# Kernel optimization log

Hardware: AMD Instinct MI355X
Metric: run time of the kernel (lower is better)

Reference implementation:

```python
import jax, jax.numpy as jnp
import numpy as np

B, S, HID = 2, 2048, 1024
H, D = 16, HID // 16  # heads, head_dim
ROPE_BASE = 10000.0


def setup_inputs() -> dict:
    key = jax.random.key(0)
    k1, k2, k3, k4 = jax.random.split(key, 4)
    scale = 1.0 / np.sqrt(HID)
    return {
        "hidden_states": jax.random.normal(k1, (B, S, HID), dtype=jnp.float32),
        "attention_mask": jnp.zeros((B, 1, 1, S), dtype=jnp.float32),
        "Wq": jax.random.normal(k2, (HID, HID), dtype=jnp.float32) * scale,
        "Wk": jax.random.normal(k3, (HID, HID), dtype=jnp.float32) * scale,
        "Wv": jax.random.normal(k4, (HID, HID), dtype=jnp.float32) * scale,
    }


def _rope_cos_sin(seq_len, dim, dtype):
    inv_freq = 1.0 / (ROPE_BASE ** (jnp.arange(0, dim, 2, dtype=jnp.float32) / dim))
    freqs = jnp.arange(seq_len, dtype=jnp.float32)[:, None] * inv_freq[None, :]  # (S, D/2)
    emb = jnp.concatenate([freqs, freqs], axis=-1)  # (S, D)
    return jnp.cos(emb).astype(dtype), jnp.sin(emb).astype(dtype)


def _rotate_half(x):
    x1, x2 = jnp.split(x, 2, axis=-1)
    return jnp.concatenate([-x2, x1], axis=-1)


def reference(hidden_states, attention_mask, Wq, Wk, Wv):
    b, s, _ = hidden_states.shape
    # QKV projections (no bias), split into heads: (b, H, s, D)
    def proj(W):
        return jnp.einsum('bse,de->bsd', hidden_states, W).reshape(b, s, H, D).transpose(0, 2, 1, 3)
    q, k, v = proj(Wq), proj(Wk), proj(Wv)
    # Rotary embedding on q, k over sequence positions
    cos, sin = _rope_cos_sin(s, D, hidden_states.dtype)  # (s, D)
    cos = cos[None, None]  # (1,1,s,D)
    sin = sin[None, None]
    q = q * cos + _rotate_half(q) * sin
    k = k * cos + _rotate_half(k) * sin
    # Scaled dot-product attention with additive mask
    scores = jnp.einsum('bhqd,bhkd->bhqk', q, k) / jnp.sqrt(jnp.asarray(D, hidden_states.dtype))
    scores = scores + attention_mask
    probs = jax.nn.softmax(scores, axis=-1)  # dropout p=0 (eval) -> identity
    ctx = jnp.einsum('bhqk,bhkd->bhqd', probs, v)
    return ctx.transpose(0, 2, 1, 3).reshape(b, s, H * D)
```

## Files before the change

kernel.cpp:

```cpp
#include <hip/hip_runtime.h>
#include <stdint.h>

typedef unsigned short u16;
typedef short bf16x8 __attribute__((ext_vector_type(8)));
typedef float f32x4 __attribute__((ext_vector_type(4)));

#define S_ 2048
#define HID_ 1024
#define H_ 16
#define D_ 64

#define LOG2E 1.4426950408889634f
#define SCALE_LOG2 0.18033688011112042f
#define MAXC_LOG2 11.541560327111707f

__device__ __forceinline__ u16 f2bf(float f) {
  uint32_t x = __builtin_bit_cast(uint32_t, f);
  uint32_t r = (x + 0x7fffu + ((x >> 16) & 1u)) >> 16;
  return (u16)r;
}
__device__ __forceinline__ uint32_t packbf2(float a, float b) {
  return (uint32_t)f2bf(a) | ((uint32_t)f2bf(b) << 16);
}
__device__ __forceinline__ uint32_t permpack(float a, float b) {
  return __builtin_amdgcn_perm(__builtin_bit_cast(uint32_t, b),
                               __builtin_bit_cast(uint32_t, a), 0x07060302u);
}

__device__ __forceinline__ void gl2lds16(const void* g, void* l) {
  __builtin_amdgcn_global_load_lds(
      (const __attribute__((address_space(1))) unsigned int*)g,
      (__attribute__((address_space(3))) unsigned int*)l, 16, 0, 0);
}

#define NX_ (1 << 20)
#define NW_ (1 << 18)
#define NROPE_ 65536
__global__ void prep_kernel(const float* __restrict__ X, const float* __restrict__ Wq,
                            const float* __restrict__ Wk, const float* __restrict__ Wv,
                            const float* __restrict__ mask, u16* __restrict__ Xb,
                            u16* __restrict__ Wqb, u16* __restrict__ Wkb,
                            u16* __restrict__ Wvb, float* __restrict__ cos_t,
                            float* __restrict__ sin_t, float* __restrict__ mask2) {
  int i = blockIdx.x * 256 + threadIdx.x;
  if (i < NX_ + 3 * NW_) {
    const float* src;
    u16* dst;
    int off;
    if (i < NX_) {
      src = X; dst = Xb; off = i;
    } else if (i < NX_ + NW_) {
      src = Wq; dst = Wqb; off = i - NX_;
    } else if (i < NX_ + 2 * NW_) {
      src = Wk; dst = Wkb; off = i - NX_ - NW_;
    } else {
      src = Wv; dst = Wvb; off = i - NX_ - 2 * NW_;
    }
    float4 v = ((const float4*)src)[off];
    uint2 packed;
    packed.x = packbf2(v.x, v.y);
    packed.y = packbf2(v.z, v.w);
    ((uint2*)dst)[off] = packed;
  } else if (i < NX_ + 3 * NW_ + NROPE_) {
    int t = i - (NX_ + 3 * NW_);
    int s = t >> 5, j = t & 31;
    float invf = powf(10000.0f, -(float)j * (1.0f / 32.0f));
    float ang = (float)s * invf;
    cos_t[t] = cosf(ang);
    sin_t[t] = sinf(ang);
  } else {
    int t = i - (NX_ + 3 * NW_ + NROPE_);
    mask2[t] = fmaf(mask[t], LOG2E, -MAXC_LOG2);
  }
}

__global__ __launch_bounds__(256) void qkv_gemm_kernel(
    const u16* __restrict__ X, const u16* __restrict__ Wq, const u16* __restrict__ Wk,
    const u16* __restrict__ Wv, const float* __restrict__ cos_t,
    const float* __restrict__ sin_t, u16* __restrict__ Q, u16* __restrict__ K,
    u16* __restrict__ Vt) {
  __shared__ char smem[65536];
  int tid = threadIdx.x;
  int lane = tid & 63, wave = tid >> 6;
  int wm = wave >> 1, wn = wave & 1;
  int quad = lane >> 4, l16 = lane & 15;
  int which = blockIdx.x >> 3;
  int nbase = (blockIdx.x & 7) * 128;
  int mbase = blockIdx.y * 128;
  const u16* W = (which == 0) ? Wq : (which == 1) ? Wk : Wv;

#pragma unroll
  for (int it = 0; it < 4; ++it) {
    int i = it * 256 + tid;
    int r = i >> 3, gs = i & 7, gsrc = gs ^ (r & 7);
    gl2lds16(X + (size_t)(mbase + r) * HID_ + gsrc * 8, smem + i * 16);
    gl2lds16(W + (size_t)(nbase + r) * HID_ + gsrc * 8, smem + 32768 + i * 16);
  }

  f32x4 acc[4][4] = {};

  for (int kk = 0; kk < 16; ++kk) {
    char* As = smem + (kk & 1) * 16384;
    char* Bs = smem + 32768 + (kk & 1) * 16384;
    __syncthreads();

    if (kk < 15) {
      int k0n = (kk + 1) * 64;
      char* An = smem + ((kk + 1) & 1) * 16384;
      char* Bn = smem + 32768 + ((kk + 1) & 1) * 16384;
#pragma unroll
      for (int it = 0; it < 4; ++it) {
        int i = it * 256 + tid;
        int r = i >> 3, gs = i & 7, gsrc = gs ^ (r & 7);
        gl2lds16(X + (size_t)(mbase + r) * HID_ + k0n + gsrc * 8, An + i * 16);
        gl2lds16(W + (size_t)(nbase + r) * HID_ + k0n + gsrc * 8, Bn + i * 16);
      }
    }

#pragma unroll
    for (int kh = 0; kh < 2; ++kh) {
      bf16x8 afrag[4], bfrag[4];
#pragma unroll
      for (int i4 = 0; i4 < 4; ++i4) {
        int r = wm * 64 + i4 * 16 + l16;
        int L = r * 8 + ((kh * 4 + quad) ^ (r & 7));
        afrag[i4] = *(const bf16x8*)(As + L * 16);
      }
#pragma unroll
      for (int j4 = 0; j4 < 4; ++j4) {
        int r = wn * 64 + j4 * 16 + l16;
        int L = r * 8 + ((kh * 4 + quad) ^ (r & 7));
        bfrag[j4] = *(const bf16x8*)(Bs + L * 16);
      }
      if (which == 2) {
#pragma unroll
        for (int i4 = 0; i4 < 4; ++i4)
#pragma unroll
          for (int j4 = 0; j4 < 4; ++j4)
            acc[i4][j4] = __builtin_amdgcn_mfma_f32_16x16x32_bf16(afrag[i4], bfrag[j4],
                                                                  acc[i4][j4], 0, 0, 0);
      } else {
#pragma unroll
        for (int i4 = 0; i4 < 4; ++i4)
#pragma unroll
          for (int j4 = 0; j4 < 4; ++j4)
            acc[i4][j4] = __builtin_amdgcn_mfma_f32_16x16x32_bf16(bfrag[j4], afrag[i4],
                                                                  acc[i4][j4], 0, 0, 0);
      }
    }
  }

  if (which == 2) {
#pragma unroll
    for (int i4 = 0; i4 < 4; ++i4)
#pragma unroll
      for (int j4 = 0; j4 < 4; ++j4) {
        int m = mbase + wm * 64 + i4 * 16 + quad * 4;
        int n = nbase + wn * 64 + j4 * 16 + l16;
        int b = m >> 11, s0 = m & 2047;
        int h = n >> 6, d = n & 63;
        uint2 pk;
        pk.x = packbf2(acc[i4][j4][0], acc[i4][j4][1]);
        pk.y = packbf2(acc[i4][j4][2], acc[i4][j4][3]);
        *(uint2*)(Vt + (((size_t)(b * H_ + h)) * D_ + d) * S_ + s0) = pk;
      }
  } else {
    u16* dst = (which == 0) ? Q : K;
#pragma unroll
    for (int i4 = 0; i4 < 4; ++i4)
#pragma unroll
      for (int j4 = 0; j4 < 2; ++j4) {
        int m = mbase + wm * 64 + i4 * 16 + l16;
        int n1 = nbase + wn * 64 + j4 * 16 + quad * 4;
        int b = m >> 11, s = m & 2047;
        int h = n1 >> 6, d1 = n1 & 63;
        float4 c4 = *(const float4*)(cos_t + s * 32 + d1);
        float4 s4 = *(const float4*)(sin_t + s * 32 + d1);
        float y1[4], y2[4];
#pragma unroll
        for (int r = 0; r < 4; ++r) {
          float cr = ((const float*)&c4)[r], sr = ((const float*)&s4)[r];
          float x1 = acc[i4][j4][r], x2 = acc[i4][j4 + 2][r];
          y1[r] = x1 * cr - x2 * sr;
          y2[r] = x2 * cr + x1 * sr;
        }
        size_t base = ((size_t)(b * H_ + h) * S_ + s) * D_;
        uint2 p1, p2;
        p1.x = packbf2(y1[0], y1[1]);
        p1.y = packbf2(y1[2], y1[3]);
        p2.x = packbf2(y2[0], y2[1]);
        p2.y = packbf2(y2[2], y2[3]);
        *(uint2*)(dst + base + d1) = p1;
        *(uint2*)(dst + base + d1 + 32) = p2;
      }
  }
}

__device__ __forceinline__ void pv_step(const char* Pr, const char* Vp, int quad, int l16,
                                        const bf16x8& ones, f32x4* o, f32x4& lacc) {
  bf16x8 p[2];
#pragma unroll
  for (int kh = 0; kh < 2; ++kh) {
    int c0 = kh * 8 + quad * 2;
    union { uint2 u[2]; bf16x8 v; } cv;
    cv.u[0] = *(const uint2*)(Pr + l16 * 128 + ((c0) ^ l16) * 8);
    cv.u[1] = *(const uint2*)(Pr + l16 * 128 + ((c0 + 1) ^ l16) * 8);
    p[kh] = cv.v;
  }
  lacc = __builtin_amdgcn_mfma_f32_16x16x32_bf16(p[0], ones, lacc, 0, 0, 0);
  lacc = __builtin_amdgcn_mfma_f32_16x16x32_bf16(p[1], ones, lacc, 0, 0, 0);
#pragma unroll
  for (int jd = 0; jd < 4; ++jd) {
    int r = jd * 16 + l16;
#pragma unroll
    for (int kh = 0; kh < 2; ++kh) {
      int L = r * 8 + ((kh * 4 + quad) ^ (r & 7));
      bf16x8 vf = *(const bf16x8*)(Vp + L * 16);
      o[jd] = __builtin_amdgcn_mfma_f32_16x16x32_bf16(p[kh], vf, o[jd], 0, 0, 0);
    }
  }
}

__global__ __launch_bounds__(512, 4) void flash_kernel(
    const u16* __restrict__ Q, const u16* __restrict__ K, const u16* __restrict__ Vt,
    const float* __restrict__ mask2, float* __restrict__ out) {
  __shared__ char smem[65536];
  int tid = threadIdx.x, wave = tid >> 6;
  int lane = tid & 63;
  int quad = lane >> 4, l16 = lane & 15;
  int bh = blockIdx.y, b = bh >> 4, h = bh & 15;
  int qbase = blockIdx.x * 128;
  int qw = qbase + wave * 16;
  char* Pw = smem + 49152 + wave * 2048;
  const float* m2row = mask2 + b * S_;
  const u16* Kbase = K + (size_t)bh * S_ * D_;
  const u16* Vbase = Vt + (size_t)bh * D_ * S_;

  bf16x8 qfrag[2];
  {
    const u16* qp = Q + ((size_t)bh * S_ + qw + l16) * D_ + quad * 8;
    qfrag[0] = *(const bf16x8*)qp;
    qfrag[1] = *(const bf16x8*)(qp + 32);
  }
  bf16x8 ones;
#pragma unroll
  for (int j = 0; j < 8; ++j) ones[j] = (short)0x3f80;

  f32x4 o[4] = {};
  f32x4 lacc = {};

  {
    int i = tid;
    int r = i >> 3, gs = i & 7, gsrc = gs ^ (r & 7);
    gl2lds16(Kbase + (size_t)r * D_ + gsrc * 8, smem + i * 16);
    gl2lds16(Vbase + (size_t)r * S_ + gsrc * 8, smem + 8192 + i * 16);
  }
  float4 mv[4];
#pragma unroll
  for (int jt = 0; jt < 4; ++jt) mv[jt] = *(const float4*)(m2row + jt * 16 + quad * 4);

  for (int kt = 0; kt < 32; ++kt) {
    char* Ks = smem + (kt % 3) * 16384;
    __syncthreads();

    if (kt < 31) {
      char* Kn = smem + ((kt + 1) % 3) * 16384;
      char* Vn = Kn + 8192;
      int nb = (kt + 1) * 64;
      int i = tid;
      int r = i >> 3, gs = i & 7, gsrc = gs ^ (r & 7);
      gl2lds16(Kbase + (size_t)(nb + r) * D_ + gsrc * 8, Kn + i * 16);
      gl2lds16(Vbase + (size_t)r * S_ + nb + gsrc * 8, Vn + i * 16);
    }

    if (kt > 0) {
      const char* Vp = smem + ((kt - 1) % 3) * 16384 + 8192;
      pv_step(Pw, Vp, quad, l16, ones, o, lacc);
    }

    f32x4 s[4] = {};
#pragma unroll
    for (int jt = 0; jt < 4; ++jt) {
      int r = jt * 16 + l16;
#pragma unroll
      for (int kh = 0; kh < 2; ++kh) {
        int L = r * 8 + ((kh * 4 + quad) ^ (r & 7));
        bf16x8 kf = *(const bf16x8*)(Ks + L * 16);
        s[jt] = __builtin_amdgcn_mfma_f32_16x16x32_bf16(kf, qfrag[kh], s[jt], 0, 0, 0);
      }
    }

#pragma unroll
    for (int jt = 0; jt < 4; ++jt) {
      float pf[4];
#pragma unroll
      for (int r = 0; r < 4; ++r) {
        float mvr = ((const float*)&mv[jt])[r];
        pf[r] = __builtin_amdgcn_exp2f(fmaf(s[jt][r], SCALE_LOG2, mvr));
      }
      uint2 pk;
      pk.x = permpack(pf[0], pf[1]);
      pk.y = permpack(pf[2], pf[3]);
      int chunk = (jt * 4 + quad) ^ l16;
      *(uint2*)(Pw + l16 * 128 + chunk * 8) = pk;
    }

    if (kt < 31) {
#pragma unroll
      for (int jt = 0; jt < 4; ++jt)
        mv[jt] = *(const float4*)(m2row + (kt + 1) * 64 + jt * 16 + quad * 4);
    }
  }

  pv_step(Pw, smem + 16384 + 8192, quad, l16, ones, o, lacc);

  float inv[4];
#pragma unroll
  for (int r = 0; r < 4; ++r) inv[r] = 1.0f / lacc[r];
#pragma unroll
  for (int jd = 0; jd < 4; ++jd) {
#pragma unroll
    for (int r = 0; r < 4; ++r) {
      int d = jd * 16 + l16;
      int q = qw + quad * 4 + r;
      out[(((size_t)b * S_ + q) * H_ + h) * D_ + d] = o[jd][r] * inv[r];
    }
  }
}

extern "C" void kernel_launch(void* const* d_in, const int* in_sizes, int n_in,
                              void* d_out, int out_size, void* d_ws, size_t ws_size,
                              hipStream_t stream) {
  const float* hid = (const float*)d_in[0];
  const float* mask = (const float*)d_in[1];
  const float* Wq = (const float*)d_in[2];
  const float* Wk = (const float*)d_in[3];
  const float* Wv = (const float*)d_in[4];
  float* out = (float*)d_out;
  char* ws = (char*)d_ws;

  u16* Xbf = (u16*)ws;
  u16* Wqb = (u16*)(ws + (8u << 20));
  u16* Wkb = (u16*)(ws + (10u << 20));
  u16* Wvb = (u16*)(ws + (12u << 20));
  u16* Qb = (u16*)(ws + (14u << 20));
  u16* Kb = (u16*)(ws + (22u << 20));
  u16* Vtb = (u16*)(ws + (30u << 20));
  float* cos_t = (float*)(ws + (38u << 20));
  float* sin_t = (float*)(ws + (38u << 20) + (256u << 10));
  float* mask2 = (float*)(ws + (38u << 20) + (512u << 10));

  prep_kernel<<<7440, 256, 0, stream>>>(hid, Wq, Wk, Wv, mask, Xbf, Wqb, Wkb, Wvb,
                                        cos_t, sin_t, mask2);
  qkv_gemm_kernel<<<dim3(24, 32), 256, 0, stream>>>(Xbf, Wqb, Wkb, Wvb, cos_t, sin_t,
                                                    Qb, Kb, Vtb);
  flash_kernel<<<dim3(16, 32), 512, 0, stream>>>(Qb, Kb, Vtb, mask2, out);
}
```

Baseline: 175.2 us.

## Process two 16-row query blocks per wave to reuse K/V fragments

Halves the flash-attention block to 256 threads (4 waves) and gives each wave 32 query rows, split into two 16-row sub-blocks. Each K and V fragment read from LDS now feeds two MFMAs, which halves LDS reads per unit of compute. Cooperative global-to-LDS loads are split into two halves per thread. The cost is more registers per wave and fewer waves per block, which can reduce latency hiding and occupancy.

```diff
diff --git a/kernel.cpp b/kernel.cpp
--- a/kernel.cpp
+++ b/kernel.cpp
@@ -196,19 +196,23 @@
   }
 }
 
-__device__ __forceinline__ void pv_step(const char* Pr, const char* Vp, int quad, int l16,
-                                        const bf16x8& ones, f32x4* o, f32x4& lacc) {
-  bf16x8 p[2];
-#pragma unroll
-  for (int kh = 0; kh < 2; ++kh) {
-    int c0 = kh * 8 + quad * 2;
-    union { uint2 u[2]; bf16x8 v; } cv;
-    cv.u[0] = *(const uint2*)(Pr + l16 * 128 + ((c0) ^ l16) * 8);
-    cv.u[1] = *(const uint2*)(Pr + l16 * 128 + ((c0 + 1) ^ l16) * 8);
-    p[kh] = cv.v;
-  }
-  lacc = __builtin_amdgcn_mfma_f32_16x16x32_bf16(p[0], ones, lacc, 0, 0, 0);
-  lacc = __builtin_amdgcn_mfma_f32_16x16x32_bf16(p[1], ones, lacc, 0, 0, 0);
+__device__ __forceinline__ void pv_step(const char* Pw, const char* Vp, int quad, int l16,
+                                        const bf16x8& ones, f32x4 (*o)[4], f32x4* lacc) {
+  bf16x8 p[2][2];
+#pragma unroll
+  for (int qb = 0; qb < 2; ++qb) {
+    const char* Pr = Pw + qb * 2048;
+#pragma unroll
+    for (int kh = 0; kh < 2; ++kh) {
+      int c0 = kh * 8 + quad * 2;
+      union { uint2 u[2]; bf16x8 v; } cv;
+      cv.u[0] = *(const uint2*)(Pr + l16 * 128 + ((c0) ^ l16) * 8);
+      cv.u[1] = *(const uint2*)(Pr + l16 * 128 + ((c0 + 1) ^ l16) * 8);
+      p[qb][kh] = cv.v;
+    }
+    lacc[qb] = __builtin_amdgcn_mfma_f32_16x16x32_bf16(p[qb][0], ones, lacc[qb], 0, 0, 0);
+    lacc[qb] = __builtin_amdgcn_mfma_f32_16x16x32_bf16(p[qb][1], ones, lacc[qb], 0, 0, 0);
+  }
 #pragma unroll
   for (int jd = 0; jd < 4; ++jd) {
     int r = jd * 16 + l16;
@@ -216,12 +220,13 @@
     for (int kh = 0; kh < 2; ++kh) {
       int L = r * 8 + ((kh * 4 + quad) ^ (r & 7));
       bf16x8 vf = *(const bf16x8*)(Vp + L * 16);
-      o[jd] = __builtin_amdgcn_mfma_f32_16x16x32_bf16(p[kh], vf, o[jd], 0, 0, 0);
-    }
-  }
-}
-
-__global__ __launch_bounds__(512, 4) void flash_kernel(
+      o[0][jd] = __builtin_amdgcn_mfma_f32_16x16x32_bf16(p[0][kh], vf, o[0][jd], 0, 0, 0);
+      o[1][jd] = __builtin_amdgcn_mfma_f32_16x16x32_bf16(p[1][kh], vf, o[1][jd], 0, 0, 0);
+    }
+  }
+}
+
+__global__ __launch_bounds__(256, 2) void flash_kernel(
     const u16* __restrict__ Q, const u16* __restrict__ K, const u16* __restrict__ Vt,
     const float* __restrict__ mask2, float* __restrict__ out) {
   __shared__ char smem[65536];
@@ -230,27 +235,29 @@
   int quad = lane >> 4, l16 = lane & 15;
   int bh = blockIdx.y, b = bh >> 4, h = bh & 15;
   int qbase = blockIdx.x * 128;
-  int qw = qbase + wave * 16;
-  char* Pw = smem + 49152 + wave * 2048;
+  int qw = qbase + wave * 32;
+  char* Pw = smem + 49152 + wave * 4096;
   const float* m2row = mask2 + b * S_;
   const u16* Kbase = K + (size_t)bh * S_ * D_;
   const u16* Vbase = Vt + (size_t)bh * D_ * S_;
 
-  bf16x8 qfrag[2];
-  {
-    const u16* qp = Q + ((size_t)bh * S_ + qw + l16) * D_ + quad * 8;
-    qfrag[0] = *(const bf16x8*)qp;
-    qfrag[1] = *(const bf16x8*)(qp + 32);
+  bf16x8 qfrag[2][2];
+#pragma unroll
+  for (int qb = 0; qb < 2; ++qb) {
+    const u16* qp = Q + ((size_t)bh * S_ + qw + qb * 16 + l16) * D_ + quad * 8;
+    qfrag[qb][0] = *(const bf16x8*)qp;
+    qfrag[qb][1] = *(const bf16x8*)(qp + 32);
   }
   bf16x8 ones;
 #pragma unroll
   for (int j = 0; j < 8; ++j) ones[j] = (short)0x3f80;
 
-  f32x4 o[4] = {};
-  f32x4 lacc = {};
-
-  {
-    int i = tid;
+  f32x4 o[2][4] = {};
+  f32x4 lacc[2] = {};
+
+#pragma unroll
+  for (int half = 0; half < 2; ++half) {
+    int i = half * 256 + tid;
     int r = i >> 3, gs = i & 7, gsrc = gs ^ (r & 7);
     gl2lds16(Kbase + (size_t)r * D_ + gsrc * 8, smem + i * 16);
     gl2lds16(Vbase + (size_t)r * S_ + gsrc * 8, smem + 8192 + i * 16);
@@ -267,10 +274,13 @@
       char* Kn = smem + ((kt + 1) % 3) * 16384;
       char* Vn = Kn + 8192;
       int nb = (kt + 1) * 64;
-      int i = tid;
-      int r = i >> 3, gs = i & 7, gsrc = gs ^ (r & 7);
-      gl2lds16(Kbase + (size_t)(nb + r) * D_ + gsrc * 8, Kn + i * 16);
-      gl2lds16(Vbase + (size_t)r * S_ + nb + gsrc * 8, Vn + i * 16);
+#pragma unroll
+      for (int half = 0; half < 2; ++half) {
+        int i = half * 256 + tid;
+        int r = i >> 3, gs = i & 7, gsrc = gs ^ (r & 7);
+        gl2lds16(Kbase + (size_t)(nb + r) * D_ + gsrc * 8, Kn + i * 16);
+        gl2lds16(Vbase + (size_t)r * S_ + nb + gsrc * 8, Vn + i * 16);
+      }
     }
 
     if (kt > 0) {
@@ -278,7 +288,7 @@
       pv_step(Pw, Vp, quad, l16, ones, o, lacc);
     }
 
-    f32x4 s[4] = {};
+    f32x4 s[2][4] = {};
 #pragma unroll
     for (int jt = 0; jt < 4; ++jt) {
       int r = jt * 16 + l16;
@@ -286,24 +296,27 @@
       for (int kh = 0; kh < 2; ++kh) {
         int L = r * 8 + ((kh * 4 + quad) ^ (r & 7));
         bf16x8 kf = *(const bf16x8*)(Ks + L * 16);
-        s[jt] = __builtin_amdgcn_mfma_f32_16x16x32_bf16(kf, qfrag[kh], s[jt], 0, 0, 0);
-      }
-    }
-
-#pragma unroll
-    for (int jt = 0; jt < 4; ++jt) {
-      float pf[4];
-#pragma unroll
-      for (int r = 0; r < 4; ++r) {
-        float mvr = ((const float*)&mv[jt])[r];
-        pf[r] = __builtin_amdgcn_exp2f(fmaf(s[jt][r], SCALE_LOG2, mvr));
-      }
-      uint2 pk;
-      pk.x = permpack(pf[0], pf[1]);
-      pk.y = permpack(pf[2], pf[3]);
-      int chunk = (jt * 4 + quad) ^ l16;
-      *(uint2*)(Pw + l16 * 128 + chunk * 8) = pk;
-    }
+        s[0][jt] = __builtin_amdgcn_mfma_f32_16x16x32_bf16(kf, qfrag[0][kh], s[0][jt], 0, 0, 0);
+        s[1][jt] = __builtin_amdgcn_mfma_f32_16x16x32_bf16(kf, qfrag[1][kh], s[1][jt], 0, 0, 0);
+      }
+    }
+
+#pragma unroll
+    for (int qb = 0; qb < 2; ++qb)
+#pragma unroll
+      for (int jt = 0; jt < 4; ++jt) {
+        float pf[4];
+#pragma unroll
+        for (int r = 0; r < 4; ++r) {
+          float mvr = ((const float*)&mv[jt])[r];
+          pf[r] = __builtin_amdgcn_exp2f(fmaf(s[qb][jt][r], SCALE_LOG2, mvr));
+        }
+        uint2 pk;
+        pk.x = permpack(pf[0], pf[1]);
+        pk.y = permpack(pf[2], pf[3]);
+        int chunk = (jt * 4 + quad) ^ l16;
+        *(uint2*)(Pw + qb * 2048 + l16 * 128 + chunk * 8) = pk;
+      }
 
     if (kt < 31) {
 #pragma unroll
@@ -314,18 +327,22 @@
 
   pv_step(Pw, smem + 16384 + 8192, quad, l16, ones, o, lacc);
 
-  float inv[4];
-#pragma unroll
-  for (int r = 0; r < 4; ++r) inv[r] = 1.0f / lacc[r];
-#pragma unroll
-  for (int jd = 0; jd < 4; ++jd) {
-#pragma unroll
-    for (int r = 0; r < 4; ++r) {
-      int d = jd * 16 + l16;
-      int q = qw + quad * 4 + r;
-      out[(((size_t)b * S_ + q) * H_ + h) * D_ + d] = o[jd][r] * inv[r];
-    }
-  }
+  float inv[2][4];
+#pragma unroll
+  for (int qb = 0; qb < 2; ++qb)
+#pragma unroll
+    for (int r = 0; r < 4; ++r) inv[qb][r] = 1.0f / lacc[qb][r];
+#pragma unroll
+  for (int qb = 0; qb < 2; ++qb)
+#pragma unroll
+    for (int jd = 0; jd < 4; ++jd) {
+#pragma unroll
+      for (int r = 0; r < 4; ++r) {
+        int d = jd * 16 + l16;
+        int q = qw + qb * 16 + quad * 4 + r;
+        out[(((size_t)b * S_ + q) * H_ + h) * D_ + d] = o[qb][jd][r] * inv[qb][r];
+      }
+    }
 }
 
 extern "C" void kernel_launch(void* const* d_in, const int* in_sizes, int n_in,
@@ -354,5 +371,5 @@
                                         cos_t, sin_t, mask2);
   qkv_gemm_kernel<<<dim3(24, 32), 256, 0, stream>>>(Xbf, Wqb, Wkb, Wvb, cos_t, sin_t,
                                                     Qb, Kb, Vtb);
-  flash_kernel<<<dim3(16, 32), 512, 0, stream>>>(Qb, Kb, Vtb, mask2, out);
-}
+  flash_kernel<<<dim3(16, 32), 256, 0, stream>>>(Qb, Kb, Vtb, mask2, out);
+}
```

New measurement: 170.1 us. 2.9% less time.
